# Kernel tuning notes

Hardware: AMD Instinct MI355X
Metric: run time of the kernel (lower is better)

Reference implementation:

```python
import jax, jax.numpy as jnp
import numpy as np
import math

DIM = 256
NUM_HEADS = 8
WS = 7  # window side (7x7 windows)


def setup_inputs() -> dict:
    key = jax.random.key(0)
    ks = jax.random.split(key, 7)
    B, H, W, C = 32, 56, 56, DIM
    x = jax.random.normal(ks[0], (B, H, W, C), dtype=jnp.float32)
    s = 1.0 / math.sqrt(C)
    Wq = jax.random.normal(ks[1], (C, C), dtype=jnp.float32) * s
    bq = jax.random.normal(ks[2], (C,), dtype=jnp.float32) * 0.01
    Wk = jax.random.normal(ks[3], (C, C), dtype=jnp.float32) * s
    bk = jax.random.normal(ks[4], (C,), dtype=jnp.float32) * 0.01
    Wv = jax.random.normal(ks[5], (C, C), dtype=jnp.float32) * s
    bv = jax.random.normal(ks[6], (C,), dtype=jnp.float32) * 0.01
    return {"x": x, "Wq": Wq, "bq": bq, "Wk": Wk, "bk": bk, "Wv": Wv, "bv": bv}


def _window_partition(x):
    # [B, H, W, C] -> [B, nW, WS*WS, C]
    B, H, W, C = x.shape
    x = x.reshape(B, H // WS, WS, W // WS, WS, C)
    x = x.transpose(0, 1, 3, 2, 4, 5)
    return x.reshape(B, (H // WS) * (W // WS), WS * WS, C)


def reference(x, Wq, bq, Wk, bk, Wv, bv):
    B, H, W, C = x.shape
    hd = C // NUM_HEADS
    win = _window_partition(x)              # [B, nW, T, C], T = 49
    nW, T = win.shape[1], win.shape[2]

    def proj(Wm, bm):
        # nn.Linear: y = x @ W^T + b; split heads -> [B, nW, T, h, hd]
        y = jnp.einsum('bwtc,dc->bwtd', win, Wm) + bm
        return y.reshape(B, nW, T, NUM_HEADS, hd)

    q = proj(Wq, bq)
    k = proj(Wk, bk)
    v = proj(Wv, bv)

    # NOTE: original scales by sqrt(self.dimension) (full dim), not head_dim.
    scale = 1.0 / math.sqrt(C)
    logits = jnp.einsum('bwqhd,bwkhd->bwhqk', q, k) * scale  # [B, nW, h, T, T]
    attn = jax.nn.softmax(logits, axis=-1)
    out = jnp.einsum('bwhqk,bwkhd->bwqhd', attn, v)          # [B, nW, T, h, hd]
    return out.reshape(B, nW, T, C)
```

## Files before the change

### kernel.cpp

```cpp
#include <hip/hip_runtime.h>
#include <hip/hip_bf16.h>

typedef __bf16 bf16_t;
typedef __bf16 bf16x8 __attribute__((ext_vector_type(8)));
typedef float  f32x4  __attribute__((ext_vector_type(4)));

#define XP 264
#define QP 72
#define VP 72
#define PP 72
#define SCL 0.09016844f

__device__ inline bf16x8 cvt8(f32x4 a, f32x4 b) {
    bf16x8 r;
    r[0]=(bf16_t)a[0]; r[1]=(bf16_t)a[1]; r[2]=(bf16_t)a[2]; r[3]=(bf16_t)a[3];
    r[4]=(bf16_t)b[0]; r[5]=(bf16_t)b[1]; r[6]=(bf16_t)b[2]; r[7]=(bf16_t)b[3];
    return r;
}

__global__ __launch_bounds__(256)
void wcvt_kernel(const float* __restrict__ Wq, const float* __restrict__ Wk,
                 const float* __restrict__ Wv, bf16_t* __restrict__ o)
{
    int e = (blockIdx.x * 256 + threadIdx.x) * 8;
    const float* src = (e < 65536) ? (Wq + e)
                     : (e < 131072 ? (Wk + (e - 65536)) : (Wv + (e - 131072)));
    f32x4 f0 = *(const f32x4*)src;
    f32x4 f1 = *(const f32x4*)(src + 4);
    *(bf16x8*)(o + e) = cvt8(f0, f1);
}

__global__ __launch_bounds__(256, 3)
void swin_win_attn(const float* __restrict__ x,
                   const bf16_t* __restrict__ Wb,
                   const float* __restrict__ bq, const float* __restrict__ bk,
                   const float* __restrict__ bv,
                   float* __restrict__ out)
{
    __shared__ __attribute__((aligned(16))) bf16_t smem[49 * XP + 2 * 64 * QP + 64 * VP];
    bf16_t* sX  = smem;
    bf16_t* sQ  = smem + 49 * XP;
    bf16_t* sK  = sQ + 64 * QP;
    bf16_t* sVT = sK + 64 * QP;

    const int tid  = threadIdx.x;
    const int wv   = tid >> 6;
    const int lane = tid & 63;
    const int l15  = lane & 15;
    const int quad = lane >> 4;

    const int win = blockIdx.x;
    const int b  = win >> 6;
    const int w  = win & 63;
    const int wy = w >> 3;
    const int wx = w & 7;
    const float* xw = x + (((b * 56) + wy * 7) * 56 + wx * 7) * 256;

    f32x4 la[7], lb[7];
    #pragma unroll
    for (int k = 0; k < 6; ++k) {
        int idx = k * 256 + tid, row = idx >> 5, cv = idx & 31;
        int ty = row / 7, tx = row - ty * 7;
        const float* src = xw + (ty * 56 + tx) * 256 + cv * 8;
        la[k] = *(const f32x4*)src;
        lb[k] = *(const f32x4*)(src + 4);
    }
    if (tid < 32) {
        const float* src = xw + (6 * 56 + 6) * 256 + tid * 8;
        la[6] = *(const f32x4*)src;
        lb[6] = *(const f32x4*)(src + 4);
    }
    bf16x8 xreg[3];
    #pragma unroll
    for (int k = 0; k < 6; ++k) {
        int idx = k * 256 + tid, row = idx >> 5, cv = idx & 31;
        bf16x8 c = cvt8(la[k], lb[k]);
        if (k < 3) xreg[k] = c;
        *(bf16x8*)&sX[row * XP + cv * 8] = c;
    }
    if (tid < 32)
        *(bf16x8*)&sX[48 * XP + tid * 8] = cvt8(la[6], lb[6]);

    const int lcol = wv * 16 + l15;
    int dglob = lcol;
    const bf16_t* wbase = Wb + dglob * 256 + quad * 8;
    bf16x8 wq[8];
    #pragma unroll
    for (int ks = 0; ks < 8; ++ks) wq[ks] = *(const bf16x8*)(wbase + ks * 32);
    float biq = bq[dglob], bik = bk[dglob], biv = bv[dglob];

    bf16x8 vone;
    #pragma unroll
    for (int j = 0; j < 8; ++j) vone[j] = (bf16_t)1.0f;

    __syncthreads();

    #pragma unroll 1
    for (int g = 0; g < 4; ++g) {
        {
            f32x4 acc[4];
            #pragma unroll
            for (int mt = 0; mt < 4; ++mt) acc[mt] = f32x4{0.f, 0.f, 0.f, 0.f};
            #pragma unroll
            for (int ks = 0; ks < 8; ++ks) {
                #pragma unroll
                for (int mt = 0; mt < 4; ++mt) {
                    bf16x8 a = *(const bf16x8*)&sX[(mt * 16 + l15) * XP + ks * 32 + quad * 8];
                    acc[mt] = __builtin_amdgcn_mfma_f32_16x16x32_bf16(a, wq[ks], acc[mt], 0, 0, 0);
                }
            }
            #pragma unroll
            for (int mt = 0; mt < 4; ++mt)
                #pragma unroll
                for (int r = 0; r < 4; ++r) {
                    int row = mt * 16 + quad * 4 + r;
                    sQ[row * QP + lcol] = (bf16_t)(acc[mt][r] + biq);
                }
        }
        {
            bf16x8 wt[8];
            #pragma unroll
            for (int ks = 0; ks < 8; ++ks) wt[ks] = *(const bf16x8*)(wbase + 2 * 65536 + ks * 32);
            f32x4 acc[4];
            #pragma unroll
            for (int mt = 0; mt < 4; ++mt) acc[mt] = f32x4{0.f, 0.f, 0.f, 0.f};
            #pragma unroll
            for (int ks = 0; ks < 8; ++ks) {
                #pragma unroll
                for (int mt = 0; mt < 4; ++mt) {
                    bf16x8 a = *(const bf16x8*)&sX[(mt * 16 + l15) * XP + ks * 32 + quad * 8];
                    acc[mt] = __builtin_amdgcn_mfma_f32_16x16x32_bf16(a, wt[ks], acc[mt], 0, 0, 0);
                }
            }
            #pragma unroll
            for (int mt = 0; mt < 4; ++mt)
                #pragma unroll
                for (int r = 0; r < 4; ++r) {
                    int row = mt * 16 + quad * 4 + r;
                    sVT[lcol * VP + row] = (row < 49) ? (bf16_t)(acc[mt][r] + biv) : (bf16_t)0.0f;
                }
        }
        {
            bf16x8 wt[8];
            #pragma unroll
            for (int ks = 0; ks < 8; ++ks) wt[ks] = *(const bf16x8*)(wbase + 65536 + ks * 32);
            f32x4 acc[4];
            #pragma unroll
            for (int mt = 0; mt < 4; ++mt) acc[mt] = f32x4{0.f, 0.f, 0.f, 0.f};
            #pragma unroll
            for (int ks = 0; ks < 8; ++ks) {
                #pragma unroll
                for (int mt = 0; mt < 4; ++mt) {
                    bf16x8 a = *(const bf16x8*)&sX[(mt * 16 + l15) * XP + ks * 32 + quad * 8];
                    acc[mt] = __builtin_amdgcn_mfma_f32_16x16x32_bf16(a, wt[ks], acc[mt], 0, 0, 0);
                }
            }
            #pragma unroll
            for (int mt = 0; mt < 4; ++mt)
                #pragma unroll
                for (int r = 0; r < 4; ++r) {
                    int row = mt * 16 + quad * 4 + r;
                    sK[row * QP + lcol] = (bf16_t)(acc[mt][r] + bik);
                }
        }
        __syncthreads();

        bf16_t* sP = &sX[wv * 16 * PP];
        #pragma unroll
        for (int hs = 0; hs < 2; ++hs) {
            const int hc = hs * 32;
            bf16x8 aq = *(const bf16x8*)&sQ[(wv * 16 + l15) * QP + hc + quad * 8];
            f32x4 sc[4];
            #pragma unroll
            for (int tj = 0; tj < 4; ++tj) {
                bf16x8 kb = *(const bf16x8*)&sK[(tj * 16 + l15) * QP + hc + quad * 8];
                f32x4 z = {0.f, 0.f, 0.f, 0.f};
                sc[tj] = __builtin_amdgcn_mfma_f32_16x16x32_bf16(aq, kb, z, 0, 0, 0);
            }
            #pragma unroll
            for (int r = 0; r < 4; ++r) {
                float p0 = __builtin_amdgcn_exp2f(sc[0][r] * SCL);
                float p1 = __builtin_amdgcn_exp2f(sc[1][r] * SCL);
                float p2 = __builtin_amdgcn_exp2f(sc[2][r] * SCL);
                float p3 = (l15 == 0) ? __builtin_amdgcn_exp2f(sc[3][r] * SCL) : 0.0f;
                int pr = (quad * 4 + r) * PP;
                sP[pr + l15]      = (bf16_t)p0;
                sP[pr + 16 + l15] = (bf16_t)p1;
                sP[pr + 32 + l15] = (bf16_t)p2;
                sP[pr + 48 + l15] = (bf16_t)p3;
            }
            f32x4 o0 = {0.f,0.f,0.f,0.f}, o1 = {0.f,0.f,0.f,0.f}, lsum = {0.f,0.f,0.f,0.f};
            #pragma unroll
            for (int ks = 0; ks < 2; ++ks) {
                bf16x8 ap = *(const bf16x8*)&sP[l15 * PP + ks * 32 + quad * 8];
                bf16x8 b0 = *(const bf16x8*)&sVT[(hc + l15) * VP + ks * 32 + quad * 8];
                bf16x8 b1 = *(const bf16x8*)&sVT[(hc + 16 + l15) * VP + ks * 32 + quad * 8];
                o0   = __builtin_amdgcn_mfma_f32_16x16x32_bf16(ap, b0,   o0,   0, 0, 0);
                o1   = __builtin_amdgcn_mfma_f32_16x16x32_bf16(ap, b1,   o1,   0, 0, 0);
                lsum = __builtin_amdgcn_mfma_f32_16x16x32_bf16(ap, vone, lsum, 0, 0, 0);
            }
            const int h = g * 2 + hs;
            #pragma unroll
            for (int r = 0; r < 4; ++r) {
                int t = wv * 16 + quad * 4 + r;
                if (t < 49) {
                    float rinv = __builtin_amdgcn_rcpf(lsum[r]);
                    long off = (long)(win * 49 + t) * 256 + h * 32 + l15;
                    out[off]      = o0[r] * rinv;
                    out[off + 16] = o1[r] * rinv;
                }
            }
        }
        __syncthreads();

        if (g < 3) {
            {
                int row = tid >> 5, cv = tid & 31;
                *(bf16x8*)&sX[row * XP + cv * 8] = xreg[0];
            }
            {
                int idx = 256 + tid, row = idx >> 5, cv = idx & 31;
                *(bf16x8*)&sX[row * XP + cv * 8] = xreg[1];
            }
            if (tid < 64) {
                int row = 16 + (tid >> 5), cv = tid & 31;
                *(bf16x8*)&sX[row * XP + cv * 8] = xreg[2];
            }
            dglob += 64;
            wbase += 64 * 256;
            #pragma unroll
            for (int ks = 0; ks < 8; ++ks) wq[ks] = *(const bf16x8*)(wbase + ks * 32);
            biq = bq[dglob]; bik = bk[dglob]; biv = bv[dglob];
            __syncthreads();
        }
    }
}

extern "C" void kernel_launch(void* const* d_in, const int* in_sizes, int n_in,
                              void* d_out, int out_size, void* d_ws, size_t ws_size,
                              hipStream_t stream) {
    const float* x  = (const float*)d_in[0];
    const float* Wq = (const float*)d_in[1];
    const float* bq = (const float*)d_in[2];
    const float* Wk = (const float*)d_in[3];
    const float* bk = (const float*)d_in[4];
    const float* Wv = (const float*)d_in[5];
    const float* bv = (const float*)d_in[6];
    float* out = (float*)d_out;
    bf16_t* Wb = (bf16_t*)d_ws;
    (void)in_sizes; (void)n_in; (void)out_size; (void)ws_size;

    hipLaunchKernelGGL(wcvt_kernel, dim3(96), dim3(256), 0, stream, Wq, Wk, Wv, Wb);
    hipLaunchKernelGGL(swin_win_attn, dim3(2048), dim3(256), 0, stream,
                       x, Wb, bq, bk, bv, out);
}
```

Measured before the change: 292.5 us.

## Use 512-thread blocks splitting QKV projection across token tiles and heads

Doubles the block to 8 waves. Each wave now projects one 16-column output slice of Q, K and V for two token tiles, fusing the three projections into a single k-loop that loads the weights in halves. In the attention phase each wave handles one query tile of one head, so both heads of a group run in parallel rather than sequentially. Q and K are computed transposed (weights as the A operand) so results are stored as bf16x4 vectors. This adds weight loads inside every group iteration and more registers per thread under the 512-thread launch bound.

```diff
diff --git a/kernel.cpp b/kernel.cpp
--- a/kernel.cpp
+++ b/kernel.cpp
@@ -2,6 +2,7 @@
 #include <hip/hip_bf16.h>
 
 typedef __bf16 bf16_t;
+typedef __bf16 bf16x4 __attribute__((ext_vector_type(4)));
 typedef __bf16 bf16x8 __attribute__((ext_vector_type(8)));
 typedef float  f32x4  __attribute__((ext_vector_type(4)));
 
@@ -30,7 +31,7 @@
     *(bf16x8*)(o + e) = cvt8(f0, f1);
 }
 
-__global__ __launch_bounds__(256, 3)
+__global__ __launch_bounds__(512, 4)
 void swin_win_attn(const float* __restrict__ x,
                    const bf16_t* __restrict__ Wb,
                    const float* __restrict__ bq, const float* __restrict__ bk,
@@ -56,10 +57,10 @@
     const int wx = w & 7;
     const float* xw = x + (((b * 56) + wy * 7) * 56 + wx * 7) * 256;
 
-    f32x4 la[7], lb[7];
+    f32x4 la[4], lb[4];
     #pragma unroll
-    for (int k = 0; k < 6; ++k) {
-        int idx = k * 256 + tid, row = idx >> 5, cv = idx & 31;
+    for (int k = 0; k < 3; ++k) {
+        int idx = k * 512 + tid, row = idx >> 5, cv = idx & 31;
         int ty = row / 7, tx = row - ty * 7;
         const float* src = xw + (ty * 56 + tx) * 256 + cv * 8;
         la[k] = *(const f32x4*)src;
@@ -67,27 +68,23 @@
     }
     if (tid < 32) {
         const float* src = xw + (6 * 56 + 6) * 256 + tid * 8;
-        la[6] = *(const f32x4*)src;
-        lb[6] = *(const f32x4*)(src + 4);
+        la[3] = *(const f32x4*)src;
+        lb[3] = *(const f32x4*)(src + 4);
     }
     bf16x8 xreg[3];
     #pragma unroll
-    for (int k = 0; k < 6; ++k) {
-        int idx = k * 256 + tid, row = idx >> 5, cv = idx & 31;
+    for (int k = 0; k < 3; ++k) {
+        int idx = k * 512 + tid, row = idx >> 5, cv = idx & 31;
         bf16x8 c = cvt8(la[k], lb[k]);
-        if (k < 3) xreg[k] = c;
+        xreg[k] = c;
         *(bf16x8*)&sX[row * XP + cv * 8] = c;
     }
     if (tid < 32)
-        *(bf16x8*)&sX[48 * XP + tid * 8] = cvt8(la[6], lb[6]);
-
-    const int lcol = wv * 16 + l15;
-    int dglob = lcol;
-    const bf16_t* wbase = Wb + dglob * 256 + quad * 8;
-    bf16x8 wq[8];
-    #pragma unroll
-    for (int ks = 0; ks < 8; ++ks) wq[ks] = *(const bf16x8*)(wbase + ks * 32);
-    float biq = bq[dglob], bik = bk[dglob], biv = bv[dglob];
+        *(bf16x8*)&sX[48 * XP + tid * 8] = cvt8(la[3], lb[3]);
+
+    const int dt = wv & 3;
+    const int th = wv >> 2;
+    const bf16_t* wb0 = Wb + (dt * 16 + l15) * 256 + quad * 8;
 
     bf16x8 vone;
     #pragma unroll
@@ -97,118 +94,101 @@
 
     #pragma unroll 1
     for (int g = 0; g < 4; ++g) {
+        const bf16_t* wbg = wb0 + g * 64 * 256;
+        f32x4 qb4 = *(const f32x4*)&bq[g * 64 + dt * 16 + quad * 4];
+        f32x4 kb4 = *(const f32x4*)&bk[g * 64 + dt * 16 + quad * 4];
+        float bvs = bv[g * 64 + dt * 16 + l15];
+
+        f32x4 accq[2], acck[2], accv[2];
+        #pragma unroll
+        for (int m = 0; m < 2; ++m) {
+            accq[m] = f32x4{0.f,0.f,0.f,0.f};
+            acck[m] = f32x4{0.f,0.f,0.f,0.f};
+            accv[m] = f32x4{0.f,0.f,0.f,0.f};
+        }
+        #pragma unroll
+        for (int half = 0; half < 2; ++half) {
+            bf16x8 wqf[4], wkf[4], wvf[4];
+            #pragma unroll
+            for (int ks = 0; ks < 4; ++ks) {
+                int kk = half * 4 + ks;
+                wqf[ks] = *(const bf16x8*)(wbg + kk * 32);
+                wkf[ks] = *(const bf16x8*)(wbg + 65536 + kk * 32);
+                wvf[ks] = *(const bf16x8*)(wbg + 131072 + kk * 32);
+            }
+            #pragma unroll
+            for (int m = 0; m < 2; ++m) {
+                int T = th * 2 + m;
+                #pragma unroll
+                for (int ks = 0; ks < 4; ++ks) {
+                    int kk = half * 4 + ks;
+                    bf16x8 a = *(const bf16x8*)&sX[(T * 16 + l15) * XP + kk * 32 + quad * 8];
+                    accq[m] = __builtin_amdgcn_mfma_f32_16x16x32_bf16(wqf[ks], a, accq[m], 0, 0, 0);
+                    acck[m] = __builtin_amdgcn_mfma_f32_16x16x32_bf16(wkf[ks], a, acck[m], 0, 0, 0);
+                    accv[m] = __builtin_amdgcn_mfma_f32_16x16x32_bf16(a, wvf[ks], accv[m], 0, 0, 0);
+                }
+            }
+        }
+        #pragma unroll
+        for (int m = 0; m < 2; ++m) {
+            int T = th * 2 + m;
+            bf16x4 pq, pk, pv;
+            #pragma unroll
+            for (int r = 0; r < 4; ++r) {
+                pq[r] = (bf16_t)(accq[m][r] + qb4[r]);
+                pk[r] = (bf16_t)(acck[m][r] + kb4[r]);
+                int tok = T * 16 + quad * 4 + r;
+                pv[r] = (tok < 49) ? (bf16_t)(accv[m][r] + bvs) : (bf16_t)0.0f;
+            }
+            *(bf16x4*)&sQ [(T * 16 + l15) * QP + dt * 16 + quad * 4] = pq;
+            *(bf16x4*)&sK [(T * 16 + l15) * QP + dt * 16 + quad * 4] = pk;
+            *(bf16x4*)&sVT[(dt * 16 + l15) * VP + T * 16 + quad * 4] = pv;
+        }
+        __syncthreads();
+
+        const int hc = th * 32;
+        bf16_t* sP = &sX[wv * 16 * PP];
+        bf16x8 aq = *(const bf16x8*)&sQ[(dt * 16 + l15) * QP + hc + quad * 8];
+        f32x4 sc[4];
+        #pragma unroll
+        for (int tj = 0; tj < 4; ++tj) {
+            bf16x8 kf = *(const bf16x8*)&sK[(tj * 16 + l15) * QP + hc + quad * 8];
+            f32x4 z = {0.f, 0.f, 0.f, 0.f};
+            sc[tj] = __builtin_amdgcn_mfma_f32_16x16x32_bf16(kf, aq, z, 0, 0, 0);
+        }
+        #pragma unroll
+        for (int tj = 0; tj < 3; ++tj) {
+            bf16x4 pp;
+            #pragma unroll
+            for (int r = 0; r < 4; ++r)
+                pp[r] = (bf16_t)__builtin_amdgcn_exp2f(sc[tj][r] * SCL);
+            *(bf16x4*)&sP[l15 * PP + tj * 16 + quad * 4] = pp;
+        }
         {
-            f32x4 acc[4];
-            #pragma unroll
-            for (int mt = 0; mt < 4; ++mt) acc[mt] = f32x4{0.f, 0.f, 0.f, 0.f};
-            #pragma unroll
-            for (int ks = 0; ks < 8; ++ks) {
-                #pragma unroll
-                for (int mt = 0; mt < 4; ++mt) {
-                    bf16x8 a = *(const bf16x8*)&sX[(mt * 16 + l15) * XP + ks * 32 + quad * 8];
-                    acc[mt] = __builtin_amdgcn_mfma_f32_16x16x32_bf16(a, wq[ks], acc[mt], 0, 0, 0);
-                }
-            }
-            #pragma unroll
-            for (int mt = 0; mt < 4; ++mt)
-                #pragma unroll
-                for (int r = 0; r < 4; ++r) {
-                    int row = mt * 16 + quad * 4 + r;
-                    sQ[row * QP + lcol] = (bf16_t)(acc[mt][r] + biq);
-                }
-        }
-        {
-            bf16x8 wt[8];
-            #pragma unroll
-            for (int ks = 0; ks < 8; ++ks) wt[ks] = *(const bf16x8*)(wbase + 2 * 65536 + ks * 32);
-            f32x4 acc[4];
-            #pragma unroll
-            for (int mt = 0; mt < 4; ++mt) acc[mt] = f32x4{0.f, 0.f, 0.f, 0.f};
-            #pragma unroll
-            for (int ks = 0; ks < 8; ++ks) {
-                #pragma unroll
-                for (int mt = 0; mt < 4; ++mt) {
-                    bf16x8 a = *(const bf16x8*)&sX[(mt * 16 + l15) * XP + ks * 32 + quad * 8];
-                    acc[mt] = __builtin_amdgcn_mfma_f32_16x16x32_bf16(a, wt[ks], acc[mt], 0, 0, 0);
-                }
-            }
-            #pragma unroll
-            for (int mt = 0; mt < 4; ++mt)
-                #pragma unroll
-                for (int r = 0; r < 4; ++r) {
-                    int row = mt * 16 + quad * 4 + r;
-                    sVT[lcol * VP + row] = (row < 49) ? (bf16_t)(acc[mt][r] + biv) : (bf16_t)0.0f;
-                }
-        }
-        {
-            bf16x8 wt[8];
-            #pragma unroll
-            for (int ks = 0; ks < 8; ++ks) wt[ks] = *(const bf16x8*)(wbase + 65536 + ks * 32);
-            f32x4 acc[4];
-            #pragma unroll
-            for (int mt = 0; mt < 4; ++mt) acc[mt] = f32x4{0.f, 0.f, 0.f, 0.f};
-            #pragma unroll
-            for (int ks = 0; ks < 8; ++ks) {
-                #pragma unroll
-                for (int mt = 0; mt < 4; ++mt) {
-                    bf16x8 a = *(const bf16x8*)&sX[(mt * 16 + l15) * XP + ks * 32 + quad * 8];
-                    acc[mt] = __builtin_amdgcn_mfma_f32_16x16x32_bf16(a, wt[ks], acc[mt], 0, 0, 0);
-                }
-            }
-            #pragma unroll
-            for (int mt = 0; mt < 4; ++mt)
-                #pragma unroll
-                for (int r = 0; r < 4; ++r) {
-                    int row = mt * 16 + quad * 4 + r;
-                    sK[row * QP + lcol] = (bf16_t)(acc[mt][r] + bik);
-                }
-        }
-        __syncthreads();
-
-        bf16_t* sP = &sX[wv * 16 * PP];
-        #pragma unroll
-        for (int hs = 0; hs < 2; ++hs) {
-            const int hc = hs * 32;
-            bf16x8 aq = *(const bf16x8*)&sQ[(wv * 16 + l15) * QP + hc + quad * 8];
-            f32x4 sc[4];
-            #pragma unroll
-            for (int tj = 0; tj < 4; ++tj) {
-                bf16x8 kb = *(const bf16x8*)&sK[(tj * 16 + l15) * QP + hc + quad * 8];
-                f32x4 z = {0.f, 0.f, 0.f, 0.f};
-                sc[tj] = __builtin_amdgcn_mfma_f32_16x16x32_bf16(aq, kb, z, 0, 0, 0);
-            }
-            #pragma unroll
-            for (int r = 0; r < 4; ++r) {
-                float p0 = __builtin_amdgcn_exp2f(sc[0][r] * SCL);
-                float p1 = __builtin_amdgcn_exp2f(sc[1][r] * SCL);
-                float p2 = __builtin_amdgcn_exp2f(sc[2][r] * SCL);
-                float p3 = (l15 == 0) ? __builtin_amdgcn_exp2f(sc[3][r] * SCL) : 0.0f;
-                int pr = (quad * 4 + r) * PP;
-                sP[pr + l15]      = (bf16_t)p0;
-                sP[pr + 16 + l15] = (bf16_t)p1;
-                sP[pr + 32 + l15] = (bf16_t)p2;
-                sP[pr + 48 + l15] = (bf16_t)p3;
-            }
-            f32x4 o0 = {0.f,0.f,0.f,0.f}, o1 = {0.f,0.f,0.f,0.f}, lsum = {0.f,0.f,0.f,0.f};
-            #pragma unroll
-            for (int ks = 0; ks < 2; ++ks) {
-                bf16x8 ap = *(const bf16x8*)&sP[l15 * PP + ks * 32 + quad * 8];
-                bf16x8 b0 = *(const bf16x8*)&sVT[(hc + l15) * VP + ks * 32 + quad * 8];
-                bf16x8 b1 = *(const bf16x8*)&sVT[(hc + 16 + l15) * VP + ks * 32 + quad * 8];
-                o0   = __builtin_amdgcn_mfma_f32_16x16x32_bf16(ap, b0,   o0,   0, 0, 0);
-                o1   = __builtin_amdgcn_mfma_f32_16x16x32_bf16(ap, b1,   o1,   0, 0, 0);
-                lsum = __builtin_amdgcn_mfma_f32_16x16x32_bf16(ap, vone, lsum, 0, 0, 0);
-            }
-            const int h = g * 2 + hs;
-            #pragma unroll
-            for (int r = 0; r < 4; ++r) {
-                int t = wv * 16 + quad * 4 + r;
-                if (t < 49) {
-                    float rinv = __builtin_amdgcn_rcpf(lsum[r]);
-                    long off = (long)(win * 49 + t) * 256 + h * 32 + l15;
-                    out[off]      = o0[r] * rinv;
-                    out[off + 16] = o1[r] * rinv;
-                }
+            bf16x4 pp;
+            pp[0] = (quad == 0) ? (bf16_t)__builtin_amdgcn_exp2f(sc[3][0] * SCL) : (bf16_t)0.0f;
+            pp[1] = (bf16_t)0.0f; pp[2] = (bf16_t)0.0f; pp[3] = (bf16_t)0.0f;
+            *(bf16x4*)&sP[l15 * PP + 48 + quad * 4] = pp;
+        }
+        f32x4 o0 = {0.f,0.f,0.f,0.f}, o1 = {0.f,0.f,0.f,0.f}, lsum = {0.f,0.f,0.f,0.f};
+        #pragma unroll
+        for (int ks = 0; ks < 2; ++ks) {
+            bf16x8 ap = *(const bf16x8*)&sP[l15 * PP + ks * 32 + quad * 8];
+            bf16x8 b0 = *(const bf16x8*)&sVT[(hc + l15) * VP + ks * 32 + quad * 8];
+            bf16x8 b1 = *(const bf16x8*)&sVT[(hc + 16 + l15) * VP + ks * 32 + quad * 8];
+            o0   = __builtin_amdgcn_mfma_f32_16x16x32_bf16(ap, b0,   o0,   0, 0, 0);
+            o1   = __builtin_amdgcn_mfma_f32_16x16x32_bf16(ap, b1,   o1,   0, 0, 0);
+            lsum = __builtin_amdgcn_mfma_f32_16x16x32_bf16(ap, vone, lsum, 0, 0, 0);
+        }
+        const int h = g * 2 + th;
+        #pragma unroll
+        for (int r = 0; r < 4; ++r) {
+            int t = dt * 16 + quad * 4 + r;
+            if (t < 49) {
+                float rinv = __builtin_amdgcn_rcpf(lsum[r]);
+                long off = (long)(win * 49 + t) * 256 + h * 32 + l15;
+                out[off]      = o0[r] * rinv;
+                out[off + 16] = o1[r] * rinv;
             }
         }
         __syncthreads();
@@ -219,18 +199,13 @@
                 *(bf16x8*)&sX[row * XP + cv * 8] = xreg[0];
             }
             {
-                int idx = 256 + tid, row = idx >> 5, cv = idx & 31;
+                int row = 16 + (tid >> 5), cv = tid & 31;
                 *(bf16x8*)&sX[row * XP + cv * 8] = xreg[1];
             }
-            if (tid < 64) {
-                int row = 16 + (tid >> 5), cv = tid & 31;
+            if (tid < 128) {
+                int row = 32 + (tid >> 5), cv = tid & 31;
                 *(bf16x8*)&sX[row * XP + cv * 8] = xreg[2];
             }
-            dglob += 64;
-            wbase += 64 * 256;
-            #pragma unroll
-            for (int ks = 0; ks < 8; ++ks) wq[ks] = *(const bf16x8*)(wbase + ks * 32);
-            biq = bq[dglob]; bik = bk[dglob]; biv = bv[dglob];
             __syncthreads();
         }
     }
@@ -251,6 +226,6 @@
     (void)in_sizes; (void)n_in; (void)out_size; (void)ws_size;
 
     hipLaunchKernelGGL(wcvt_kernel, dim3(96), dim3(256), 0, stream, Wq, Wk, Wv, Wb);
-    hipLaunchKernelGGL(swin_win_attn, dim3(2048), dim3(256), 0, stream,
+    hipLaunchKernelGGL(swin_win_attn, dim3(2048), dim3(512), 0, stream,
                        x, Wb, bq, bk, bv, out);
 }
```

Result: slower. 348.7 us (+19.2%).
